# Kernel optimization log

Hardware: AMD Instinct MI355X
Metric: run time of the kernel (lower is better)

The kernel has to match this reference:

```python
import jax, jax.numpy as jnp
import numpy as np

D = 1024
H = 16
DH = D // H
B = 8
T = 1024
EPS = 1e-5


def setup_inputs() -> dict:
    key = jax.random.key(0)
    ks = jax.random.split(key, 12)
    s = 0.02
    return {
        "x": jax.random.normal(ks[0], (B, T, D), dtype=jnp.float32),
        "ln1_scale": jnp.ones((D,), jnp.float32),
        "ln1_shift": jnp.zeros((D,), jnp.float32),
        "Wq": jax.random.normal(ks[1], (D, D), jnp.float32) * s,
        "Wk": jax.random.normal(ks[2], (D, D), jnp.float32) * s,
        "Wv": jax.random.normal(ks[3], (D, D), jnp.float32) * s,
        "Wo": jax.random.normal(ks[4], (D, D), jnp.float32) * s,
        "bo": jnp.zeros((D,), jnp.float32),
        "ln2_scale": jnp.ones((D,), jnp.float32),
        "ln2_shift": jnp.zeros((D,), jnp.float32),
        "W1": jax.random.normal(ks[5], (D, 4 * D), jnp.float32) * s,
        "b1": jnp.zeros((4 * D,), jnp.float32),
        "W2": jax.random.normal(ks[6], (4 * D, D), jnp.float32) * s,
        "b2": jnp.zeros((D,), jnp.float32),
    }


def _layernorm(x, scale, shift):
    mean = jnp.mean(x, axis=-1, keepdims=True)
    var = jnp.mean((x - mean) ** 2, axis=-1, keepdims=True)  # unbiased=False
    return (x - mean) * jax.lax.rsqrt(var + EPS) * scale + shift


def _gelu_tanh(x):
    c = jnp.sqrt(jnp.float32(2.0 / jnp.pi))
    return 0.5 * x * (1.0 + jnp.tanh(c * (x + 0.044715 * x ** 3)))


def reference(x, ln1_scale, ln1_shift, Wq, Wk, Wv, Wo, bo,
              ln2_scale, ln2_shift, W1, b1, W2, b2):
    b, t, d = x.shape
    x1 = _layernorm(x, ln1_scale, ln1_shift)
    # QKV projections (no bias), split heads -> (b, h, t, d_h)
    q = (x1 @ Wq).reshape(b, t, H, DH).transpose(0, 2, 1, 3)
    k = (x1 @ Wk).reshape(b, t, H, DH).transpose(0, 2, 1, 3)
    v = (x1 @ Wv).reshape(b, t, H, DH).transpose(0, 2, 1, 3)
    scores = jnp.einsum("bhqd,bhkd->bhqk", q, k) / jnp.sqrt(jnp.float32(DH))
    # original does tril then adds -inf upper-triangular mask -> standard causal mask
    causal = jnp.tril(jnp.ones((t, t), dtype=bool))
    scores = jnp.where(causal, scores, -jnp.inf)
    attn = jax.nn.softmax(scores, axis=-1)
    z = jnp.einsum("bhqk,bhkd->bhqd", attn, v)
    z = z.transpose(0, 2, 1, 3).reshape(b, t, d)
    x2 = z @ Wo + bo
    y = x2 + x
    y1 = _layernorm(y, ln2_scale, ln2_shift)
    y2 = _gelu_tanh(y1 @ W1 + b1) @ W2 + b2
    return y2 + y
```

## Files before the change

kernel.cpp:

```cpp
#include <hip/hip_runtime.h>

typedef unsigned short u16;
typedef __bf16 bf16x8 __attribute__((ext_vector_type(8)));
typedef float f32x4 __attribute__((ext_vector_type(4)));

#define D_MODEL 1024
#define NHEAD 16
#define DHEAD 64
#define BATCH 8
#define SEQ 1024
#define NROW 8192

__device__ __forceinline__ u16 f2bf(float f) {
  union { float f; unsigned int u; } a; a.f = f;
  unsigned int u = a.u;
  return (u16)((u + 0x7fffu + ((u >> 16) & 1u)) >> 16);
}

__device__ __forceinline__ float bf2f(u16 b) {
  union { unsigned int u; float f; } a; a.u = ((unsigned int)b) << 16;
  return a.f;
}

__device__ __forceinline__ float gelu_f(float x) {
  float y = 0.79788456080286535588f * (x + 0.044715f * x * x * x);
  return x / (1.0f + __expf(-2.0f * y));
}

__device__ __forceinline__ void async16(const void* gsrc, void* ldst) {
  __builtin_amdgcn_global_load_lds((__attribute__((address_space(1))) void*)gsrc,
                                   (__attribute__((address_space(3))) void*)ldst,
                                   16, 0, 0);
}

template <int N> __device__ __forceinline__ void vmwait() {
  if constexpr (N == 4)      asm volatile("s_waitcnt vmcnt(4)" ::: "memory");
  else                       asm volatile("s_waitcnt vmcnt(0)" ::: "memory");
}

__global__ __launch_bounds__(256)
void wconv4_kernel(const float* __restrict__ Wa, const float* __restrict__ Wb,
                   const float* __restrict__ Wc, const float* __restrict__ Wd,
                   u16* __restrict__ WT) {
  const float* Ws[4] = {Wa, Wb, Wc, Wd};
  const float* W = Ws[blockIdx.z];
  u16* dst = WT + (size_t)blockIdx.z * 1024 * 1024;
  __shared__ float tile[32][33];
  const int tx = threadIdx.x & 31, ty = threadIdx.x >> 5;
  const int n0 = blockIdx.x * 32, k0 = blockIdx.y * 32;
#pragma unroll
  for (int r = 0; r < 4; ++r)
    tile[ty + r * 8][tx] = W[(size_t)(k0 + ty + r * 8) * 1024 + n0 + tx];
  __syncthreads();
#pragma unroll
  for (int r = 0; r < 4; ++r)
    dst[(size_t)(n0 + ty + r * 8) * 1024 + k0 + tx] = f2bf(tile[tx][ty + r * 8]);
}

__global__ __launch_bounds__(256)
void wconv_kernel(const float* __restrict__ W, u16* __restrict__ WT, int K, int N) {
  __shared__ float tile[32][33];
  const int tx = threadIdx.x & 31, ty = threadIdx.x >> 5;
  const int n0 = blockIdx.x * 32, k0 = blockIdx.y * 32;
#pragma unroll
  for (int r = 0; r < 4; ++r)
    tile[ty + r * 8][tx] = W[(size_t)(k0 + ty + r * 8) * N + n0 + tx];
  __syncthreads();
#pragma unroll
  for (int r = 0; r < 4; ++r)
    WT[(size_t)(n0 + ty + r * 8) * K + k0 + tx] = f2bf(tile[tx][ty + r * 8]);
}

__global__ __launch_bounds__(256)
void ln_kernel(const float* __restrict__ x, const float* __restrict__ gamma,
               const float* __restrict__ beta, u16* __restrict__ out) {
  const int row = blockIdx.x, t = threadIdx.x;
  const float4 v = ((const float4*)(x + (size_t)row * D_MODEL))[t];
  float s  = v.x + v.y + v.z + v.w;
  float s2 = v.x * v.x + v.y * v.y + v.z * v.z + v.w * v.w;
#pragma unroll
  for (int off = 32; off >= 1; off >>= 1) {
    s  += __shfl_down(s, off);
    s2 += __shfl_down(s2, off);
  }
  __shared__ float red[8];
  const int w = t >> 6, l = t & 63;
  if (l == 0) { red[w] = s; red[4 + w] = s2; }
  __syncthreads();
  s  = red[0] + red[1] + red[2] + red[3];
  s2 = red[4] + red[5] + red[6] + red[7];
  const float mean = s * (1.0f / D_MODEL);
  const float var  = s2 * (1.0f / D_MODEL) - mean * mean;
  const float inv  = rsqrtf(var + 1e-5f);
  const float4 ga = ((const float4*)gamma)[t];
  const float4 be = ((const float4*)beta)[t];
  ushort4 ov;
  ov.x = f2bf((v.x - mean) * inv * ga.x + be.x);
  ov.y = f2bf((v.y - mean) * inv * ga.y + be.y);
  ov.z = f2bf((v.z - mean) * inv * ga.z + be.z);
  ov.w = f2bf((v.w - mean) * inv * ga.w + be.w);
  ((ushort4*)out)[(size_t)row * 256 + t] = ov;
}

__global__ __launch_bounds__(256)
void ln_bf16_kernel(const u16* __restrict__ x, const float* __restrict__ gamma,
                    const float* __restrict__ beta, u16* __restrict__ out) {
  const int row = blockIdx.x, t = threadIdx.x;
  const ushort4 bv = ((const ushort4*)(x + (size_t)row * D_MODEL))[t];
  float4 v;
  v.x = bf2f(bv.x); v.y = bf2f(bv.y); v.z = bf2f(bv.z); v.w = bf2f(bv.w);
  float s  = v.x + v.y + v.z + v.w;
  float s2 = v.x * v.x + v.y * v.y + v.z * v.z + v.w * v.w;
#pragma unroll
  for (int off = 32; off >= 1; off >>= 1) {
    s  += __shfl_down(s, off);
    s2 += __shfl_down(s2, off);
  }
  __shared__ float red[8];
  const int w = t >> 6, l = t & 63;
  if (l == 0) { red[w] = s; red[4 + w] = s2; }
  __syncthreads();
  s  = red[0] + red[1] + red[2] + red[3];
  s2 = red[4] + red[5] + red[6] + red[7];
  const float mean = s * (1.0f / D_MODEL);
  const float var  = s2 * (1.0f / D_MODEL) - mean * mean;
  const float inv  = rsqrtf(var + 1e-5f);
  const float4 ga = ((const float4*)gamma)[t];
  const float4 be = ((const float4*)beta)[t];
  ushort4 ov;
  ov.x = f2bf((v.x - mean) * inv * ga.x + be.x);
  ov.y = f2bf((v.y - mean) * inv * ga.y + be.y);
  ov.z = f2bf((v.z - mean) * inv * ga.z + be.z);
  ov.w = f2bf((v.w - mean) * inv * ga.w + be.w);
  ((ushort4*)out)[(size_t)row * 256 + t] = ov;
}

#define MODE_QK 0
#define MODE_VT 1
#define MODE_YRES 2
#define MODE_GELU 3
#define MODE_OUT 4

template <int MODE, int NBUF>
__global__ __launch_bounds__(256, 4)
void gemm_bt(const u16* __restrict__ A, const u16* __restrict__ BT,
             const float* __restrict__ bias, const float* __restrict__ resid,
             void* __restrict__ outp, int M, int N, int K) {
  __shared__ u16 sA[NBUF][128 * 32];
  __shared__ u16 sB[NBUF][128 * 32];
  const int t = threadIdx.x;
  const int w = t >> 6, l = t & 63;
  const int c = l & 15, g = l >> 4;
  const int wr = w >> 1, wc = w & 1;
  const int bm = blockIdx.x, bn = blockIdx.y;

  f32x4 acc[4][4] = {};

  const char* Ab = (const char*)(A + (size_t)bm * 128 * K);
  const char* Bb = (const char*)(BT + (size_t)bn * 128 * K);
  const size_t ldb = (size_t)K * 2;
  const int srow = t >> 2;
  const int scolb = (t & 3) * 16;
  const int ldsoff = w * 1024;

  auto stage = [&](int buf, int k0) {
#pragma unroll
    for (int i = 0; i < 2; ++i) {
      async16(Ab + (size_t)(srow + i * 64) * ldb + (size_t)k0 * 2 + scolb,
              (char*)sA[buf] + i * 4096 + ldsoff);
      async16(Bb + (size_t)(srow + i * 64) * ldb + (size_t)k0 * 2 + scolb,
              (char*)sB[buf] + i * 4096 + ldsoff);
    }
  };

  auto compute = [&](int cur) {
    bf16x8 af[4], bfr[4];
#pragma unroll
    for (int m = 0; m < 4; ++m)
      af[m] = *(const bf16x8*)&sA[cur][(wr * 64 + m * 16 + c) * 32 + g * 8];
#pragma unroll
    for (int n = 0; n < 4; ++n)
      bfr[n] = *(const bf16x8*)&sB[cur][(wc * 64 + n * 16 + c) * 32 + g * 8];
#pragma unroll
    for (int m = 0; m < 4; ++m)
#pragma unroll
      for (int n = 0; n < 4; ++n)
        acc[m][n] = __builtin_amdgcn_mfma_f32_16x16x32_bf16(af[m], bfr[n], acc[m][n], 0, 0, 0);
  };

  const int nt = K >> 5;

  if constexpr (NBUF == 2) {
    stage(0, 0);
    vmwait<0>();
    __builtin_amdgcn_s_barrier();
    for (int it = 0; it < nt; ++it) {
      const int cur = it & 1;
      if (it + 1 < nt) stage(cur ^ 1, (it + 1) << 5);
      compute(cur);
      vmwait<0>();
      __builtin_amdgcn_s_barrier();
    }
  } else {
    stage(0, 0);
    stage(1, 32);
    for (int it = 0; it < nt; ++it) {
      const int cur = it % 3;
      if (it + 1 < nt) vmwait<4>(); else vmwait<0>();
      __builtin_amdgcn_s_barrier();
      if (it + 2 < nt) stage((it + 2) % 3, (it + 2) << 5);
      compute(cur);
    }
  }

#pragma unroll
  for (int m = 0; m < 4; ++m) {
    const int r0 = bm * 128 + wr * 64 + m * 16 + g * 4;
#pragma unroll
    for (int n = 0; n < 4; ++n) {
      const int cc = bn * 128 + wc * 64 + n * 16 + c;
#pragma unroll
      for (int i = 0; i < 4; ++i) {
        const int r = r0 + i;
        const float v = acc[m][n][i];
        if constexpr (MODE == MODE_QK) {
          ((u16*)outp)[(((size_t)(r >> 10) * NHEAD + (cc >> 6)) * SEQ + (r & 1023)) * DHEAD + (cc & 63)] = f2bf(v);
        } else if constexpr (MODE == MODE_VT) {
          ((u16*)outp)[(((size_t)(r >> 10) * NHEAD + (cc >> 6)) * DHEAD + (cc & 63)) * SEQ + (r & 1023)] = f2bf(v);
        } else if constexpr (MODE == MODE_YRES) {
          const size_t idx = (size_t)r * N + cc;
          ((u16*)outp)[idx] = f2bf(v + bias[cc] + resid[idx]);
        } else if constexpr (MODE == MODE_OUT) {
          const size_t idx = (size_t)r * N + cc;
          ((float*)outp)[idx] = v + bias[cc] + bf2f(((const u16*)resid)[idx]);
        } else {
          const size_t idx = (size_t)r * N + cc;
          ((u16*)outp)[idx] = f2bf(gelu_f(v + bias[cc]));
        }
      }
    }
  }
}

__global__ __launch_bounds__(256, 3)
void attn_kernel(const u16* __restrict__ q, const u16* __restrict__ k,
                 const u16* __restrict__ vT, u16* __restrict__ z) {
  __shared__ u16 sK[2][64 * 64];
  __shared__ u16 sV[2][64 * 64];
  __shared__ u16 pb[4][32 * 64];

  const int t = threadIdx.x, w = t >> 6, l = t & 63;
  const int c = l & 15, g = l >> 4;
  const int bh = blockIdx.y;
  const int qb0 = blockIdx.x * 128;
  const int qw0 = qb0 + w * 32;

  const u16* qbase = q  + (size_t)bh * SEQ * DHEAD;
  const u16* kbase = k  + (size_t)bh * SEQ * DHEAD;
  const u16* vbase = vT + (size_t)bh * DHEAD * SEQ;

  bf16x8 qf[2][2];
#pragma unroll
  for (int j = 0; j < 2; ++j)
#pragma unroll
    for (int hh = 0; hh < 2; ++hh)
      qf[j][hh] = *(const bf16x8*)&qbase[(size_t)(qw0 + j * 16 + c) * DHEAD + hh * 32 + g * 8];

  f32x4 o[4][2] = {};
  float m[2]  = {-3.0e38f, -3.0e38f};
  float ls[2] = {0.0f, 0.0f};

  const int r8 = l >> 3, ch = l & 7;
  const int sw16 = (ch ^ r8) * 16;

  auto stage = [&](int buf, int kt) {
    const int kb0 = kt * 64;
#pragma unroll
    for (int i = 0; i < 2; ++i) {
      const int row = w * 8 + i * 32 + r8;
      async16((const char*)kbase + (size_t)(kb0 + row) * 128 + sw16,
              (char*)sK[buf] + w * 1024 + i * 4096);
      async16((const char*)vbase + (size_t)row * (SEQ * 2) + (size_t)kb0 * 2 + sw16,
              (char*)sV[buf] + w * 1024 + i * 4096);
    }
  };

  const int nkt = blockIdx.x * 2 + 2;
  stage(0, 0);

  for (int kt = 0; kt < nkt; ++kt) {
    const int cur = kt & 1;
    if (kt + 1 < nkt) {
      stage(cur ^ 1, kt + 1);
      asm volatile("s_waitcnt vmcnt(4)" ::: "memory");
    } else {
      asm volatile("s_waitcnt vmcnt(0)" ::: "memory");
    }
    __builtin_amdgcn_s_barrier();

    const int kb0 = kt * 64;
    if (kb0 < qw0 + 32) {
      const u16* sKc = sK[cur];
      const u16* sVc = sV[cur];
      const int cx = c & 7;

      f32x4 st[4][2];
#pragma unroll
      for (int s = 0; s < 4; ++s) {
        const int row = s * 16 + c;
        bf16x8 kf0 = *(const bf16x8*)&sKc[row * 64 + ((0 + g) ^ cx) * 8];
        bf16x8 kf1 = *(const bf16x8*)&sKc[row * 64 + ((4 + g) ^ cx) * 8];
#pragma unroll
        for (int j = 0; j < 2; ++j) {
          f32x4 z4 = {};
          z4 = __builtin_amdgcn_mfma_f32_16x16x32_bf16(kf0, qf[j][0], z4, 0, 0, 0);
          z4 = __builtin_amdgcn_mfma_f32_16x16x32_bf16(kf1, qf[j][1], z4, 0, 0, 0);
          st[s][j] = z4;
        }
      }

      const bool full = (kb0 + 64 <= qw0 + 1);
      float tmax[2] = {-3.0e38f, -3.0e38f};
#pragma unroll
      for (int s = 0; s < 4; ++s)
#pragma unroll
        for (int j = 0; j < 2; ++j)
#pragma unroll
          for (int i = 0; i < 4; ++i) {
            float vsc = st[s][j][i] * 0.125f;
            if (!full) {
              const int key = kb0 + s * 16 + g * 4 + i;
              vsc = (key <= qw0 + j * 16 + c) ? vsc : -1.0e30f;
            }
            st[s][j][i] = vsc;
            tmax[j] = fmaxf(tmax[j], vsc);
          }
#pragma unroll
      for (int j = 0; j < 2; ++j) {
        tmax[j] = fmaxf(tmax[j], __shfl_xor(tmax[j], 16));
        tmax[j] = fmaxf(tmax[j], __shfl_xor(tmax[j], 32));
      }
      float mnew[2], sc[2], psum[2];
#pragma unroll
      for (int j = 0; j < 2; ++j) {
        mnew[j] = fmaxf(m[j], tmax[j]);
        sc[j]   = __expf(m[j] - mnew[j]);
        psum[j] = 0.0f;
      }
#pragma unroll
      for (int s = 0; s < 4; ++s)
#pragma unroll
        for (int j = 0; j < 2; ++j)
#pragma unroll
          for (int i = 0; i < 4; ++i) {
            const float pv = __expf(st[s][j][i] - mnew[j]);
            st[s][j][i] = pv;
            psum[j] += pv;
          }
#pragma unroll
      for (int j = 0; j < 2; ++j) {
        psum[j] += __shfl_xor(psum[j], 16);
        psum[j] += __shfl_xor(psum[j], 32);
        ls[j] = ls[j] * sc[j] + psum[j];
        m[j]  = mnew[j];
#pragma unroll
        for (int d = 0; d < 4; ++d) o[d][j] = o[d][j] * sc[j];
      }

      u16* pw = pb[w];
#pragma unroll
      for (int s = 0; s < 4; ++s)
#pragma unroll
        for (int j = 0; j < 2; ++j) {
          const int row = j * 16 + c;
          const int swz = (s * 2 + (g >> 1)) ^ cx;
          ushort4 pv4;
          pv4.x = f2bf(st[s][j][0]); pv4.y = f2bf(st[s][j][1]);
          pv4.z = f2bf(st[s][j][2]); pv4.w = f2bf(st[s][j][3]);
          *(ushort4*)&pw[row * 64 + swz * 8 + (g & 1) * 4] = pv4;
        }

      bf16x8 pf[2][2];
#pragma unroll
      for (int j = 0; j < 2; ++j)
#pragma unroll
        for (int ks = 0; ks < 2; ++ks)
          pf[j][ks] = *(const bf16x8*)&pw[(j * 16 + c) * 64 + ((ks * 4 + g) ^ cx) * 8];

#pragma unroll
      for (int d = 0; d < 4; ++d) {
        const int vrow = d * 16 + c;
#pragma unroll
        for (int ks = 0; ks < 2; ++ks) {
          bf16x8 vf = *(const bf16x8*)&sVc[vrow * 64 + ((ks * 4 + g) ^ cx) * 8];
#pragma unroll
          for (int j = 0; j < 2; ++j)
            o[d][j] = __builtin_amdgcn_mfma_f32_16x16x32_bf16(vf, pf[j][ks], o[d][j], 0, 0, 0);
        }
      }
    }
    __builtin_amdgcn_s_barrier();
  }

  const int b = bh >> 4, h = bh & 15;
#pragma unroll
  for (int j = 0; j < 2; ++j) {
    const float inv = 1.0f / ls[j];
    const int qrow = qw0 + j * 16 + c;
    u16* zr = z + ((size_t)b * SEQ + qrow) * D_MODEL + h * DHEAD;
#pragma unroll
    for (int d = 0; d < 4; ++d) {
      ushort4 ov;
      ov.x = f2bf(o[d][j][0] * inv); ov.y = f2bf(o[d][j][1] * inv);
      ov.z = f2bf(o[d][j][2] * inv); ov.w = f2bf(o[d][j][3] * inv);
      *(ushort4*)&zr[d * 16 + g * 4] = ov;
    }
  }
}

extern "C" void kernel_launch(void* const* d_in, const int* in_sizes, int n_in,
                              void* d_out, int out_size, void* d_ws, size_t ws_size,
                              hipStream_t stream) {
  (void)in_sizes; (void)n_in; (void)out_size; (void)ws_size;
  const float* x   = (const float*)d_in[0];
  const float* g1  = (const float*)d_in[1];
  const float* s1  = (const float*)d_in[2];
  const float* Wq  = (const float*)d_in[3];
  const float* Wk  = (const float*)d_in[4];
  const float* Wv  = (const float*)d_in[5];
  const float* Wo  = (const float*)d_in[6];
  const float* bo  = (const float*)d_in[7];
  const float* g2  = (const float*)d_in[8];
  const float* s2  = (const float*)d_in[9];
  const float* W1  = (const float*)d_in[10];
  const float* b1  = (const float*)d_in[11];
  const float* W2  = (const float*)d_in[12];
  const float* b2  = (const float*)d_in[13];
  float* out = (float*)d_out;
  char* ws = (char*)d_ws;
  const size_t MB = 1024 * 1024;

  u16* wqT = (u16*)(ws + 0 * MB);
  u16* wkT = (u16*)(ws + 2 * MB);
  u16* wvT = (u16*)(ws + 4 * MB);
  u16* woT = (u16*)(ws + 6 * MB);
  u16* w1T = (u16*)(ws + 8 * MB);
  u16* w2T = (u16*)(ws + 16 * MB);
  u16* x1  = (u16*)(ws + 24 * MB);
  u16* qb  = (u16*)(ws + 40 * MB);
  u16* kb  = (u16*)(ws + 56 * MB);
  u16* vb  = (u16*)(ws + 72 * MB);
  u16* hb  = (u16*)(ws + 24 * MB);
  u16* zb  = (u16*)(ws + 88 * MB);
  u16* y1  = (u16*)(ws + 88 * MB);
  u16* yb  = (u16*)(ws + 104 * MB);

  wconv4_kernel<<<dim3(32, 32, 4), 256, 0, stream>>>(Wq, Wk, Wv, Wo, wqT);
  wconv_kernel<<<dim3(128, 32), 256, 0, stream>>>(W1, w1T, 1024, 4096);
  wconv_kernel<<<dim3(32, 128), 256, 0, stream>>>(W2, w2T, 4096, 1024);
  ln_kernel<<<NROW, 256, 0, stream>>>(x, g1, s1, x1);
  gemm_bt<MODE_QK, 3><<<dim3(64, 8), 256, 0, stream>>>(x1, wqT, nullptr, nullptr, qb, NROW, 1024, 1024);
  gemm_bt<MODE_QK, 3><<<dim3(64, 8), 256, 0, stream>>>(x1, wkT, nullptr, nullptr, kb, NROW, 1024, 1024);
  gemm_bt<MODE_VT, 3><<<dim3(64, 8), 256, 0, stream>>>(x1, wvT, nullptr, nullptr, vb, NROW, 1024, 1024);
  attn_kernel<<<dim3(8, 128), 256, 0, stream>>>(qb, kb, vb, zb);
  gemm_bt<MODE_YRES, 3><<<dim3(64, 8), 256, 0, stream>>>(zb, woT, bo, x, yb, NROW, 1024, 1024);
  ln_bf16_kernel<<<NROW, 256, 0, stream>>>(yb, g2, s2, y1);
  gemm_bt<MODE_GELU, 2><<<dim3(64, 32), 256, 0, stream>>>(y1, w1T, b1, nullptr,
                                                          hb, NROW, 4096, 1024);
  gemm_bt<MODE_OUT, 3><<<dim3(64, 8), 256, 0, stream>>>(hb, w2T, b2, (const float*)yb,
                                                        out, NROW, 1024, 4096);
}
```

Before: 403.5 us.

## Use K=64 double-buffered GEMM with XOR-swizzled LDS for N=1024 projections

Adds a gemm64 kernel that stages 64-wide K slices per iteration into double-buffered LDS, using an XOR swizzle on 16-byte chunks to avoid bank conflicts. It replaces the 3-buffer K=32 GEMM for the QKV, output-projection and W2 GEMMs, halving the number of barriers and wait points per K. The GELU GEMM keeps the 2-buffer K=32 path. The larger LDS footprint lowers occupancy to 2 blocks per CU, which may reduce latency hiding.

```diff
diff --git a/kernel.cpp b/kernel.cpp
--- a/kernel.cpp
+++ b/kernel.cpp
@@ -31,11 +31,6 @@
   __builtin_amdgcn_global_load_lds((__attribute__((address_space(1))) void*)gsrc,
                                    (__attribute__((address_space(3))) void*)ldst,
                                    16, 0, 0);
-}
-
-template <int N> __device__ __forceinline__ void vmwait() {
-  if constexpr (N == 4)      asm volatile("s_waitcnt vmcnt(4)" ::: "memory");
-  else                       asm volatile("s_waitcnt vmcnt(0)" ::: "memory");
 }
 
 __global__ __launch_bounds__(256)
@@ -141,78 +136,11 @@
 #define MODE_GELU 3
 #define MODE_OUT 4
 
-template <int MODE, int NBUF>
-__global__ __launch_bounds__(256, 4)
-void gemm_bt(const u16* __restrict__ A, const u16* __restrict__ BT,
-             const float* __restrict__ bias, const float* __restrict__ resid,
-             void* __restrict__ outp, int M, int N, int K) {
-  __shared__ u16 sA[NBUF][128 * 32];
-  __shared__ u16 sB[NBUF][128 * 32];
-  const int t = threadIdx.x;
-  const int w = t >> 6, l = t & 63;
-  const int c = l & 15, g = l >> 4;
-  const int wr = w >> 1, wc = w & 1;
-  const int bm = blockIdx.x, bn = blockIdx.y;
-
-  f32x4 acc[4][4] = {};
-
-  const char* Ab = (const char*)(A + (size_t)bm * 128 * K);
-  const char* Bb = (const char*)(BT + (size_t)bn * 128 * K);
-  const size_t ldb = (size_t)K * 2;
-  const int srow = t >> 2;
-  const int scolb = (t & 3) * 16;
-  const int ldsoff = w * 1024;
-
-  auto stage = [&](int buf, int k0) {
-#pragma unroll
-    for (int i = 0; i < 2; ++i) {
-      async16(Ab + (size_t)(srow + i * 64) * ldb + (size_t)k0 * 2 + scolb,
-              (char*)sA[buf] + i * 4096 + ldsoff);
-      async16(Bb + (size_t)(srow + i * 64) * ldb + (size_t)k0 * 2 + scolb,
-              (char*)sB[buf] + i * 4096 + ldsoff);
-    }
-  };
-
-  auto compute = [&](int cur) {
-    bf16x8 af[4], bfr[4];
-#pragma unroll
-    for (int m = 0; m < 4; ++m)
-      af[m] = *(const bf16x8*)&sA[cur][(wr * 64 + m * 16 + c) * 32 + g * 8];
-#pragma unroll
-    for (int n = 0; n < 4; ++n)
-      bfr[n] = *(const bf16x8*)&sB[cur][(wc * 64 + n * 16 + c) * 32 + g * 8];
-#pragma unroll
-    for (int m = 0; m < 4; ++m)
-#pragma unroll
-      for (int n = 0; n < 4; ++n)
-        acc[m][n] = __builtin_amdgcn_mfma_f32_16x16x32_bf16(af[m], bfr[n], acc[m][n], 0, 0, 0);
-  };
-
-  const int nt = K >> 5;
-
-  if constexpr (NBUF == 2) {
-    stage(0, 0);
-    vmwait<0>();
-    __builtin_amdgcn_s_barrier();
-    for (int it = 0; it < nt; ++it) {
-      const int cur = it & 1;
-      if (it + 1 < nt) stage(cur ^ 1, (it + 1) << 5);
-      compute(cur);
-      vmwait<0>();
-      __builtin_amdgcn_s_barrier();
-    }
-  } else {
-    stage(0, 0);
-    stage(1, 32);
-    for (int it = 0; it < nt; ++it) {
-      const int cur = it % 3;
-      if (it + 1 < nt) vmwait<4>(); else vmwait<0>();
-      __builtin_amdgcn_s_barrier();
-      if (it + 2 < nt) stage((it + 2) % 3, (it + 2) << 5);
-      compute(cur);
-    }
-  }
-
+template <int MODE>
+__device__ __forceinline__ void gemm_epilogue(f32x4 (&acc)[4][4], int bm, int bn,
+                                              int wr, int wc, int c, int g,
+                                              const float* bias, const float* resid,
+                                              void* outp, int N) {
 #pragma unroll
   for (int m = 0; m < 4; ++m) {
     const int r0 = bm * 128 + wr * 64 + m * 16 + g * 4;
@@ -240,6 +168,137 @@
       }
     }
   }
+}
+
+template <int MODE>
+__global__ __launch_bounds__(256, 4)
+void gemm_bt(const u16* __restrict__ A, const u16* __restrict__ BT,
+             const float* __restrict__ bias, const float* __restrict__ resid,
+             void* __restrict__ outp, int M, int N, int K) {
+  __shared__ u16 sA[2][128 * 32];
+  __shared__ u16 sB[2][128 * 32];
+  const int t = threadIdx.x;
+  const int w = t >> 6, l = t & 63;
+  const int c = l & 15, g = l >> 4;
+  const int wr = w >> 1, wc = w & 1;
+  const int bm = blockIdx.x, bn = blockIdx.y;
+
+  f32x4 acc[4][4] = {};
+
+  const char* Ab = (const char*)(A + (size_t)bm * 128 * K);
+  const char* Bb = (const char*)(BT + (size_t)bn * 128 * K);
+  const size_t ldb = (size_t)K * 2;
+  const int srow = t >> 2;
+  const int scolb = (t & 3) * 16;
+  const int ldsoff = w * 1024;
+
+  auto stage = [&](int buf, int k0) {
+#pragma unroll
+    for (int i = 0; i < 2; ++i) {
+      async16(Ab + (size_t)(srow + i * 64) * ldb + (size_t)k0 * 2 + scolb,
+              (char*)sA[buf] + i * 4096 + ldsoff);
+      async16(Bb + (size_t)(srow + i * 64) * ldb + (size_t)k0 * 2 + scolb,
+              (char*)sB[buf] + i * 4096 + ldsoff);
+    }
+  };
+
+  stage(0, 0);
+  asm volatile("s_waitcnt vmcnt(0)" ::: "memory");
+  __builtin_amdgcn_s_barrier();
+
+  const int nt = K >> 5;
+  for (int it = 0; it < nt; ++it) {
+    const int cur = it & 1;
+    if (it + 1 < nt) stage(cur ^ 1, (it + 1) << 5);
+    bf16x8 af[4], bfr[4];
+#pragma unroll
+    for (int m = 0; m < 4; ++m)
+      af[m] = *(const bf16x8*)&sA[cur][(wr * 64 + m * 16 + c) * 32 + g * 8];
+#pragma unroll
+    for (int n = 0; n < 4; ++n)
+      bfr[n] = *(const bf16x8*)&sB[cur][(wc * 64 + n * 16 + c) * 32 + g * 8];
+#pragma unroll
+    for (int m = 0; m < 4; ++m)
+#pragma unroll
+      for (int n = 0; n < 4; ++n)
+        acc[m][n] = __builtin_amdgcn_mfma_f32_16x16x32_bf16(af[m], bfr[n], acc[m][n], 0, 0, 0);
+    asm volatile("s_waitcnt vmcnt(0)" ::: "memory");
+    __builtin_amdgcn_s_barrier();
+  }
+
+  gemm_epilogue<MODE>(acc, bm, bn, wr, wc, c, g, bias, resid, outp, N);
+}
+
+template <int MODE>
+__global__ __launch_bounds__(256, 2)
+void gemm64(const u16* __restrict__ A, const u16* __restrict__ BT,
+            const float* __restrict__ bias, const float* __restrict__ resid,
+            void* __restrict__ outp, int M, int N, int K) {
+  __shared__ u16 sA[2][128 * 64];
+  __shared__ u16 sB[2][128 * 64];
+  const int t = threadIdx.x;
+  const int w = t >> 6, l = t & 63;
+  const int c = l & 15, g = l >> 4;
+  const int wr = w >> 1, wc = w & 1;
+  const int bm = blockIdx.x, bn = blockIdx.y;
+
+  f32x4 acc[4][4] = {};
+
+  const char* Ab = (const char*)(A + (size_t)bm * 128 * K);
+  const char* Bb = (const char*)(BT + (size_t)bn * 128 * K);
+  const size_t ldb = (size_t)K * 2;
+
+  int soff[4];
+#pragma unroll
+  for (int i = 0; i < 4; ++i) {
+    const int o = i * 256 + t, row = o >> 3, ch = (o & 7) ^ (row & 7);
+    soff[i] = row * (int)ldb + ch * 16;
+  }
+
+  auto stage = [&](int buf, int k0) {
+    const int kb = k0 * 2;
+#pragma unroll
+    for (int i = 0; i < 4; ++i) {
+      async16(Ab + (size_t)(soff[i] + kb), (char*)sA[buf] + (i * 256 + t) * 16);
+      async16(Bb + (size_t)(soff[i] + kb), (char*)sB[buf] + (i * 256 + t) * 16);
+    }
+  };
+
+  stage(0, 0);
+  asm volatile("s_waitcnt vmcnt(0)" ::: "memory");
+  __builtin_amdgcn_s_barrier();
+
+  const int nt = K >> 6;
+  for (int it = 0; it < nt; ++it) {
+    const int cur = it & 1;
+    if (it + 1 < nt) stage(cur ^ 1, (it + 1) << 6);
+    bf16x8 af[4][2], bfr[4][2];
+#pragma unroll
+    for (int m = 0; m < 4; ++m) {
+      const int row = wr * 64 + m * 16 + c;
+#pragma unroll
+      for (int ks = 0; ks < 2; ++ks)
+        af[m][ks] = *(const bf16x8*)((const char*)sA[cur] + row * 128 + (((ks << 2) + g) ^ (row & 7)) * 16);
+    }
+#pragma unroll
+    for (int n = 0; n < 4; ++n) {
+      const int row = wc * 64 + n * 16 + c;
+#pragma unroll
+      for (int ks = 0; ks < 2; ++ks)
+        bfr[n][ks] = *(const bf16x8*)((const char*)sB[cur] + row * 128 + (((ks << 2) + g) ^ (row & 7)) * 16);
+    }
+#pragma unroll
+    for (int ks = 0; ks < 2; ++ks)
+#pragma unroll
+      for (int m = 0; m < 4; ++m)
+#pragma unroll
+        for (int n = 0; n < 4; ++n)
+          acc[m][n] = __builtin_amdgcn_mfma_f32_16x16x32_bf16(af[m][ks], bfr[n][ks], acc[m][n], 0, 0, 0);
+    asm volatile("s_waitcnt vmcnt(0)" ::: "memory");
+    __builtin_amdgcn_s_barrier();
+  }
+
+  gemm_epilogue<MODE>(acc, bm, bn, wr, wc, c, g, bias, resid, outp, N);
 }
 
 __global__ __launch_bounds__(256, 3)
@@ -459,14 +518,14 @@
   wconv_kernel<<<dim3(128, 32), 256, 0, stream>>>(W1, w1T, 1024, 4096);
   wconv_kernel<<<dim3(32, 128), 256, 0, stream>>>(W2, w2T, 4096, 1024);
   ln_kernel<<<NROW, 256, 0, stream>>>(x, g1, s1, x1);
-  gemm_bt<MODE_QK, 3><<<dim3(64, 8), 256, 0, stream>>>(x1, wqT, nullptr, nullptr, qb, NROW, 1024, 1024);
-  gemm_bt<MODE_QK, 3><<<dim3(64, 8), 256, 0, stream>>>(x1, wkT, nullptr, nullptr, kb, NROW, 1024, 1024);
-  gemm_bt<MODE_VT, 3><<<dim3(64, 8), 256, 0, stream>>>(x1, wvT, nullptr, nullptr, vb, NROW, 1024, 1024);
+  gemm64<MODE_QK><<<dim3(64, 8), 256, 0, stream>>>(x1, wqT, nullptr, nullptr, qb, NROW, 1024, 1024);
+  gemm64<MODE_QK><<<dim3(64, 8), 256, 0, stream>>>(x1, wkT, nullptr, nullptr, kb, NROW, 1024, 1024);
+  gemm64<MODE_VT><<<dim3(64, 8), 256, 0, stream>>>(x1, wvT, nullptr, nullptr, vb, NROW, 1024, 1024);
   attn_kernel<<<dim3(8, 128), 256, 0, stream>>>(qb, kb, vb, zb);
-  gemm_bt<MODE_YRES, 3><<<dim3(64, 8), 256, 0, stream>>>(zb, woT, bo, x, yb, NROW, 1024, 1024);
+  gemm64<MODE_YRES><<<dim3(64, 8), 256, 0, stream>>>(zb, woT, bo, x, yb, NROW, 1024, 1024);
   ln_bf16_kernel<<<NROW, 256, 0, stream>>>(yb, g2, s2, y1);
-  gemm_bt<MODE_GELU, 2><<<dim3(64, 32), 256, 0, stream>>>(y1, w1T, b1, nullptr,
-                                                          hb, NROW, 4096, 1024);
-  gemm_bt<MODE_OUT, 3><<<dim3(64, 8), 256, 0, stream>>>(hb, w2T, b2, (const float*)yb,
-                                                        out, NROW, 1024, 4096);
-}
+  gemm_bt<MODE_GELU><<<dim3(64, 32), 256, 0, stream>>>(y1, w1T, b1, nullptr,
+                                                       hb, NROW, 4096, 1024);
+  gemm64<MODE_OUT><<<dim3(64, 8), 256, 0, stream>>>(hb, w2T, b2, (const float*)yb,
+                                                    out, NROW, 1024, 4096);
+}
```

Measured after the change: 358.9 us. 1.12x faster.
